# Performance work log

Hardware: AMD Instinct MI355X
Metric: run time of the kernel (lower is better)

The kernel has to match this reference:

```python
import jax, jax.numpy as jnp
import numpy as np

BATCH, D_IN, HID, OUT = 16384, 2000, 100, 2
BN_EPS = 1e-5


def _quant_act(x, bit):
    # HAWQ QuantAct: per-tensor symmetric quantization, returns (dequantized x, scale)
    n = 2 ** (bit - 1) - 1
    s = jnp.max(jnp.abs(x)) / n
    q = jnp.clip(jnp.round(x / s), -n - 1, n)
    return q * s, s


def _quant_linear(x, p_sf, W, b, wbit=2, bbit=2):
    # HAWQ QuantLinear: INT-w GEMM with per-tensor weight scale; bias quantized
    # at scale w_s * p_sf; input assumed pre-quantized at scale p_sf.
    nw = 2 ** (wbit - 1) - 1
    w_s = jnp.max(jnp.abs(W)) / nw
    w_int = jnp.clip(jnp.round(W / w_s), -nw - 1, nw)          # INT2 weights in {-2..1}
    b_s = w_s * p_sf
    nb = 2 ** (bbit - 1)
    b_int = jnp.clip(jnp.round(b / b_s), -nb, nb - 1)
    x_int = x / p_sf                                            # integer-valued activations
    return (x_int @ w_int.T + b_int) * b_s


def setup_inputs() -> dict:
    key = jax.random.key(0)
    ks = jax.random.split(key, 5)
    return {
        "sig": jax.random.normal(ks[0], (BATCH, D_IN), dtype=jnp.float32),
        "W1": jax.random.normal(ks[1], (HID, D_IN), dtype=jnp.float32) * 0.02,
        "b1": jax.random.normal(ks[2], (HID,), dtype=jnp.float32) * 0.01,
        "W2": jax.random.normal(ks[3], (OUT, HID), dtype=jnp.float32) * 0.1,
        "b2": jax.random.normal(ks[4], (OUT,), dtype=jnp.float32) * 0.01,
        "gamma": jnp.ones((HID,), dtype=jnp.float32),
        "beta": jnp.zeros((HID,), dtype=jnp.float32),
    }


def reference(sig, W1, b1, W2, b2, gamma, beta):
    x, p_sf = _quant_act(sig, 5)                    # quant_input (5-bit)
    x = jax.nn.relu(_quant_linear(x, p_sf, W1, b1)) # linear1 (2-bit w/b) + relu
    x, p_sf = _quant_act(x, 8)                      # q_relu1 (8-bit)
    # BatchNorm1d(100) in training mode: batch stats, biased variance
    mu = jnp.mean(x, axis=0)
    var = jnp.mean((x - mu) ** 2, axis=0)
    x = (x - mu) * jax.lax.rsqrt(var + BN_EPS) * gamma + beta
    x = jax.nn.relu(_quant_linear(x, p_sf, W2, b2)) # linear2 (2-bit w/b) + relu
    x, p_sf = _quant_act(x, 8)                      # q_relu2 (8-bit)
    return x
```

## Files before the change

### kernel.cpp

```cpp
#include <hip/hip_runtime.h>
#include <hip/hip_bf16.h>
#include <stdint.h>

#define BATCH   16384
#define D_IN    2000
#define HID     100
#define OUT_DIM 2
#define BN_EPS_VAL 1e-5f

#define BK      32
#define BN_PAD  128
#define KT      63
#define W1Q_ELEMS (KT * BN_PAD * BK)

typedef float f32x4 __attribute__((ext_vector_type(4)));
typedef short bf16x8 __attribute__((ext_vector_type(8)));

#define WS_W1Q_OFF 4096
#define WS_H1_OFF  (1u << 20)
#define WS_Q2_OFF  (8u << 20)
#define WS_O2_OFF  (10u << 20)

__device__ __forceinline__ void block_atomic_maxf(float v, float* dst) {
#pragma unroll
    for (int off = 32; off > 0; off >>= 1)
        v = fmaxf(v, __shfl_xor(v, off, 64));
    __shared__ float sm[8];
    const int w = threadIdx.x >> 6;
    if ((threadIdx.x & 63) == 0) sm[w] = v;
    __syncthreads();
    if (threadIdx.x == 0) {
        const int nw = (blockDim.x + 63) >> 6;
        float m = sm[0];
        for (int i = 1; i < nw; ++i) m = fmaxf(m, sm[i]);
        atomicMax((unsigned int*)dst, __float_as_uint(m));
    }
}

__global__ __launch_bounds__(256)
void k_absmax(const float* __restrict__ sig, const float* __restrict__ W1,
              const float* __restrict__ W2, float* __restrict__ F) {
    float m = 0.0f;
    const int b = blockIdx.x;
    if (b < 2048) {
        const float4* p = (const float4*)sig;
        const int n4 = BATCH * D_IN / 4;
        for (int i = b * 256 + threadIdx.x; i < n4; i += 2048 * 256) {
            float4 v = p[i];
            m = fmaxf(m, fmaxf(fmaxf(fabsf(v.x), fabsf(v.y)),
                               fmaxf(fabsf(v.z), fabsf(v.w))));
        }
        block_atomic_maxf(m, &F[0]);
    } else if (b < 2064) {
        const float4* p = (const float4*)W1;
        const int n4 = HID * D_IN / 4;
        for (int i = (b - 2048) * 256 + threadIdx.x; i < n4; i += 16 * 256) {
            float4 v = p[i];
            m = fmaxf(m, fmaxf(fmaxf(fabsf(v.x), fabsf(v.y)),
                               fmaxf(fabsf(v.z), fabsf(v.w))));
        }
        block_atomic_maxf(m, &F[1]);
    } else {
        if (threadIdx.x < OUT_DIM * HID) m = fabsf(W2[threadIdx.x]);
        block_atomic_maxf(m, &F[2]);
    }
}

__global__ __launch_bounds__(256)
void k_prep(const float* __restrict__ W1, const float* __restrict__ b1,
            const float* __restrict__ W2, float* __restrict__ F,
            unsigned short* __restrict__ w1q) {
    const int tid = blockIdx.x * 256 + threadIdx.x;
    const float ws1 = F[1];
    if (tid < W1Q_ELEMS) {
        const int kt = tid >> 12;
        const int r  = tid & 4095;
        const int n  = r >> 5;
        const int kk = r & 31;
        const int k  = kt * 32 + kk;
        float q = 0.0f;
        if (n < HID && k < D_IN) {
            q = rintf(W1[n * D_IN + k] / ws1);
            q = fminf(fmaxf(q, -2.0f), 1.0f);
        }
        w1q[tid] = (unsigned short)(__float_as_uint(q) >> 16);
    } else if (tid < W1Q_ELEMS + HID) {
        const int h = tid - W1Q_ELEMS;
        const float s1 = F[0] / 15.0f;
        const float bs = ws1 * s1;
        F[16 + h] = fminf(fmaxf(rintf(b1[h] / bs), -2.0f), 1.0f);
    } else if (tid < W1Q_ELEMS + HID + OUT_DIM * HID) {
        const int j = tid - (W1Q_ELEMS + HID);
        const float ws2 = F[2];
        F[116 + j] = fminf(fmaxf(rintf(W2[j] / ws2), -2.0f), 1.0f);
    }
}

__global__ __launch_bounds__(512)
void k_gemm1(const float* __restrict__ sig, const unsigned short* __restrict__ w1q,
             float* __restrict__ F, float* __restrict__ h1) {
    __shared__ float red[4][16][113];
    const int tid  = threadIdx.x;
    const int lane = tid & 63;
    const int wid  = tid >> 6;
    const int rg   = wid & 3;
    const int ks   = wid >> 2;
    const float s1  = F[0] / 15.0f;
    const float bs1 = F[1] * s1;
    const int m0 = blockIdx.x * 64;

    const int fr = lane & 15;
    const int g8 = (lane >> 4) * 8;

    const float* aptr = sig + (size_t)(m0 + rg * 16 + fr) * D_IN;

    f32x4 acc[7] = {};

#pragma unroll 2
    for (int kt = ks; kt < KT; kt += 2) {
        const int k0 = kt * BK + g8;
        float4 va = make_float4(0.f, 0.f, 0.f, 0.f), vb = va;
        if (k0 < D_IN) {
            va = *(const float4*)(aptr + k0);
            vb = *(const float4*)(aptr + k0 + 4);
        }
        union { bf16x8 v; unsigned short s[8]; } A;
        {
            float q;
            q = fminf(fmaxf(rintf(va.x / s1), -16.f), 15.f); A.s[0] = (unsigned short)(__float_as_uint(q) >> 16);
            q = fminf(fmaxf(rintf(va.y / s1), -16.f), 15.f); A.s[1] = (unsigned short)(__float_as_uint(q) >> 16);
            q = fminf(fmaxf(rintf(va.z / s1), -16.f), 15.f); A.s[2] = (unsigned short)(__float_as_uint(q) >> 16);
            q = fminf(fmaxf(rintf(va.w / s1), -16.f), 15.f); A.s[3] = (unsigned short)(__float_as_uint(q) >> 16);
            q = fminf(fmaxf(rintf(vb.x / s1), -16.f), 15.f); A.s[4] = (unsigned short)(__float_as_uint(q) >> 16);
            q = fminf(fmaxf(rintf(vb.y / s1), -16.f), 15.f); A.s[5] = (unsigned short)(__float_as_uint(q) >> 16);
            q = fminf(fmaxf(rintf(vb.z / s1), -16.f), 15.f); A.s[6] = (unsigned short)(__float_as_uint(q) >> 16);
            q = fminf(fmaxf(rintf(vb.w / s1), -16.f), 15.f); A.s[7] = (unsigned short)(__float_as_uint(q) >> 16);
        }
        const unsigned short* bbase = w1q + ((size_t)kt * BN_PAD + fr) * BK + g8;
#pragma unroll
        for (int t = 0; t < 7; ++t) {
            bf16x8 b = *(const bf16x8*)(bbase + t * 16 * BK);
            acc[t] = __builtin_amdgcn_mfma_f32_16x16x32_bf16(A.v, b, acc[t], 0, 0, 0);
        }
    }

    const int rl = (lane >> 4) * 4;
    if (ks == 1) {
#pragma unroll
        for (int t = 0; t < 7; ++t)
#pragma unroll
            for (int r = 0; r < 4; ++r)
                red[rg][rl + r][t * 16 + fr] = acc[t][r];
    }
    __syncthreads();

    float lmax = 0.0f;
    if (ks == 0) {
#pragma unroll
        for (int t = 0; t < 7; ++t) {
            const int n = t * 16 + fr;
            if (n < HID) {
                const float bi = F[16 + n];
#pragma unroll
                for (int r = 0; r < 4; ++r) {
                    const int m = m0 + rg * 16 + rl + r;
                    float h = (acc[t][r] + red[rg][rl + r][n] + bi) * bs1;
                    h = fmaxf(h, 0.0f);
                    h1[(size_t)m * HID + n] = h;
                    lmax = fmaxf(lmax, h);
                }
            }
        }
    }
    block_atomic_maxf(lmax, &F[3]);
}

__global__ __launch_bounds__(256)
void k_quant_h(const float* __restrict__ h1, unsigned char* __restrict__ q2,
               const float* __restrict__ F, unsigned int* __restrict__ S1,
               unsigned int* __restrict__ S2) {
    __shared__ unsigned int ls1[HID], ls2[HID];
    if (threadIdx.x < HID) { ls1[threadIdx.x] = 0u; ls2[threadIdx.x] = 0u; }
    __syncthreads();
    const float s2 = F[3] / 127.0f;
    const int base = blockIdx.x * 25600;
#pragma unroll 4
    for (int it = 0; it < 100; ++it) {
        const int idx = base + it * 256 + threadIdx.x;
        const float h = h1[idx];
        const int q = (int)fminf(rintf(h / s2), 127.0f);
        q2[idx] = (unsigned char)q;
        const int c = idx % HID;
        atomicAdd(&ls1[c], (unsigned int)q);
        atomicAdd(&ls2[c], (unsigned int)(q * q));
    }
    __syncthreads();
    if (threadIdx.x < HID) {
        atomicAdd(&S1[threadIdx.x], ls1[threadIdx.x]);
        atomicAdd(&S2[threadIdx.x], ls2[threadIdx.x]);
    }
}

__global__ void k_bnprep(const float* __restrict__ b2, float* __restrict__ F,
                         const unsigned int* __restrict__ S1,
                         const unsigned int* __restrict__ S2) {
    const int t = threadIdx.x;
    const float s2  = F[3] / 127.0f;
    const float ws2 = F[2];
    const float bs2 = ws2 * s2;
    if (t < HID) {
        const double sd   = (double)s2;
        const double mean = sd * ((double)S1[t] / 16384.0);
        const double ex2  = sd * sd * ((double)S2[t] / 16384.0);
        const double var  = ex2 - mean * mean;
        const float varf  = (float)var;
        const float vpe   = varf + BN_EPS_VAL;
        const float rf    = (float)(1.0 / sqrt((double)vpe));
        F[320 + t] = (float)mean;
        F[420 + t] = rf;
    }
    if (t < OUT_DIM) F[920 + t] = fminf(fmaxf(rintf(b2[t] / bs2), -2.0f), 1.0f);
    if (t == 64) F[922] = bs2;
}

__global__ __launch_bounds__(64)
void k_gemm2(const unsigned char* __restrict__ q2, float* __restrict__ F,
             const float* __restrict__ gamma, const float* __restrict__ beta,
             float* __restrict__ out2) {
    __shared__ float sw[2 * HID], smu[HID], sr[HID], sg[HID], sb[HID];
    __shared__ float ssc[4];
    const int t = threadIdx.x;
    for (int i = t; i < 2 * HID; i += 64) sw[i] = F[116 + i];
    for (int i = t; i < HID; i += 64) {
        smu[i] = F[320 + i]; sr[i] = F[420 + i]; sg[i] = gamma[i]; sb[i] = beta[i];
    }
    if (t == 60) ssc[0] = F[3] / 127.0f;
    if (t == 61) ssc[1] = F[922];
    if (t == 62) ssc[2] = F[920];
    if (t == 63) ssc[3] = F[921];
    __syncthreads();
    const int row = blockIdx.x * 64 + t;
    const unsigned int* rp = (const unsigned int*)(q2 + (size_t)row * HID);
    const float s2 = ssc[0];
    float a0 = 0.0f, a1 = 0.0f;
#pragma unroll
    for (int j = 0; j < 25; ++j) {
        const unsigned int u = rp[j];
#pragma unroll
        for (int bb = 0; bb < 4; ++bb) {
            const int h = j * 4 + bb;
            const float q = (float)((u >> (8 * bb)) & 255u);
            const float x2v = q * s2;
            const float xb  = fmaf((x2v - smu[h]) * sr[h], sg[h], sb[h]);
            const float xi  = xb / s2;
            a0 = fmaf(xi, sw[h], a0);
            a1 = fmaf(xi, sw[HID + h], a1);
        }
    }
    const float o0 = fmaxf((a0 + ssc[2]) * ssc[1], 0.0f);
    const float o1 = fmaxf((a1 + ssc[3]) * ssc[1], 0.0f);
    out2[row * 2 + 0] = o0;
    out2[row * 2 + 1] = o1;
    block_atomic_maxf(fmaxf(o0, o1), &F[4]);
}

__global__ __launch_bounds__(256)
void k_final(const float* __restrict__ out2, const float* __restrict__ F,
             float* __restrict__ out) {
    const int i = blockIdx.x * 256 + threadIdx.x;
    const float s3 = F[4] / 127.0f;
    float4 v = ((const float4*)out2)[i];
    float4 r;
    r.x = fminf(fmaxf(rintf(v.x / s3), -128.f), 127.f) * s3;
    r.y = fminf(fmaxf(rintf(v.y / s3), -128.f), 127.f) * s3;
    r.z = fminf(fmaxf(rintf(v.z / s3), -128.f), 127.f) * s3;
    r.w = fminf(fmaxf(rintf(v.w / s3), -128.f), 127.f) * s3;
    ((float4*)out)[i] = r;
}

extern "C" void kernel_launch(void* const* d_in, const int* in_sizes, int n_in,
                              void* d_out, int out_size, void* d_ws, size_t ws_size,
                              hipStream_t stream) {
    const float* sig   = (const float*)d_in[0];
    const float* W1    = (const float*)d_in[1];
    const float* b1    = (const float*)d_in[2];
    const float* W2    = (const float*)d_in[3];
    const float* b2    = (const float*)d_in[4];
    const float* gamma = (const float*)d_in[5];
    const float* beta  = (const float*)d_in[6];

    float* F = (float*)d_ws;
    unsigned short* w1q = (unsigned short*)((char*)d_ws + WS_W1Q_OFF);
    float* h1           = (float*)((char*)d_ws + WS_H1_OFF);
    unsigned char* q2   = (unsigned char*)((char*)d_ws + WS_Q2_OFF);
    float* o2           = (float*)((char*)d_ws + WS_O2_OFF);
    unsigned int* S1    = (unsigned int*)(F + 520);
    unsigned int* S2    = (unsigned int*)(F + 620);

    hipMemsetAsync(d_ws, 0, 4096, stream);
    k_absmax <<<2065, 256, 0, stream>>>(sig, W1, W2, F);
    k_prep   <<<1010, 256, 0, stream>>>(W1, b1, W2, F, w1q);
    k_gemm1  <<<256,  512, 0, stream>>>(sig, w1q, F, h1);
    k_quant_h<<<64,   256, 0, stream>>>(h1, q2, F, S1, S2);
    k_bnprep <<<1,    128, 0, stream>>>(b2, F, S1, S2);
    k_gemm2  <<<256,  64,  0, stream>>>(q2, F, gamma, beta, o2);
    k_final  <<<32,   256, 0, stream>>>(o2, F, (float*)d_out);
}
```

Before: 315.9 us.

## Regrid GEMM1 with 4-way K split, fuse BN stats finalize into quant kernel

GEMM1 now uses 1024 blocks of 256 threads. Each block covers 16 rows, and its four wavefronts split K four ways, combining partial sums through shared memory. This replaces 256 blocks that each covered 64 rows with a 2-way K split, and the aim is more in-flight memory traffic while streaming the large input. The quant/stats kernel goes from 64 to 256 blocks and writes per-block partial sums. A last-block-done atomic counter then finalizes the BN mean and rstd in place, which removes the separate k_bnprep launch. GEMM2 uses 128-thread blocks. The K bound check on input loads was dropped, so the last tile reads a few floats past the row, and past the end of the buffer for the final row. Those reads multiply zero weights, but that relies on them holding finite values.

```diff
diff --git a/kernel.cpp b/kernel.cpp
--- a/kernel.cpp
+++ b/kernel.cpp
@@ -20,6 +20,8 @@
 #define WS_H1_OFF  (1u << 20)
 #define WS_Q2_OFF  (8u << 20)
 #define WS_O2_OFF  (10u << 20)
+#define WS_P1_OFF  (11u << 20)
+#define WS_P2_OFF  ((11u << 20) + 102400u)
 
 __device__ __forceinline__ void block_atomic_maxf(float v, float* dst) {
 #pragma unroll
@@ -96,34 +98,29 @@
     }
 }
 
-__global__ __launch_bounds__(512)
+__global__ __launch_bounds__(256)
 void k_gemm1(const float* __restrict__ sig, const unsigned short* __restrict__ w1q,
              float* __restrict__ F, float* __restrict__ h1) {
-    __shared__ float red[4][16][113];
+    __shared__ float red[3][16][113];
     const int tid  = threadIdx.x;
     const int lane = tid & 63;
-    const int wid  = tid >> 6;
-    const int rg   = wid & 3;
-    const int ks   = wid >> 2;
+    const int ks   = tid >> 6;
     const float s1  = F[0] / 15.0f;
     const float bs1 = F[1] * s1;
-    const int m0 = blockIdx.x * 64;
+    const int m0 = blockIdx.x * 16;
 
     const int fr = lane & 15;
     const int g8 = (lane >> 4) * 8;
 
-    const float* aptr = sig + (size_t)(m0 + rg * 16 + fr) * D_IN;
+    const float* aptr = sig + (size_t)(m0 + fr) * D_IN;
 
     f32x4 acc[7] = {};
 
 #pragma unroll 2
-    for (int kt = ks; kt < KT; kt += 2) {
+    for (int kt = ks; kt < KT; kt += 4) {
         const int k0 = kt * BK + g8;
-        float4 va = make_float4(0.f, 0.f, 0.f, 0.f), vb = va;
-        if (k0 < D_IN) {
-            va = *(const float4*)(aptr + k0);
-            vb = *(const float4*)(aptr + k0 + 4);
-        }
+        float4 va = *(const float4*)(aptr + k0);
+        float4 vb = *(const float4*)(aptr + k0 + 4);
         union { bf16x8 v; unsigned short s[8]; } A;
         {
             float q;
@@ -145,12 +142,12 @@
     }
 
     const int rl = (lane >> 4) * 4;
-    if (ks == 1) {
+    if (ks != 0) {
 #pragma unroll
         for (int t = 0; t < 7; ++t)
 #pragma unroll
             for (int r = 0; r < 4; ++r)
-                red[rg][rl + r][t * 16 + fr] = acc[t][r];
+                red[ks - 1][rl + r][t * 16 + fr] = acc[t][r];
     }
     __syncthreads();
 
@@ -163,8 +160,9 @@
                 const float bi = F[16 + n];
 #pragma unroll
                 for (int r = 0; r < 4; ++r) {
-                    const int m = m0 + rg * 16 + rl + r;
-                    float h = (acc[t][r] + red[rg][rl + r][n] + bi) * bs1;
+                    const int m = m0 + rl + r;
+                    float h = (acc[t][r] + red[0][rl + r][n] + red[1][rl + r][n]
+                               + red[2][rl + r][n] + bi) * bs1;
                     h = fmaxf(h, 0.0f);
                     h1[(size_t)m * HID + n] = h;
                     lmax = fmaxf(lmax, h);
@@ -177,16 +175,18 @@
 
 __global__ __launch_bounds__(256)
 void k_quant_h(const float* __restrict__ h1, unsigned char* __restrict__ q2,
-               const float* __restrict__ F, unsigned int* __restrict__ S1,
-               unsigned int* __restrict__ S2) {
+               float* __restrict__ F, unsigned int* __restrict__ P1,
+               unsigned int* __restrict__ P2, const float* __restrict__ b2) {
     __shared__ unsigned int ls1[HID], ls2[HID];
-    if (threadIdx.x < HID) { ls1[threadIdx.x] = 0u; ls2[threadIdx.x] = 0u; }
+    __shared__ bool amLast;
+    const int t = threadIdx.x;
+    if (t < HID) { ls1[t] = 0u; ls2[t] = 0u; }
     __syncthreads();
     const float s2 = F[3] / 127.0f;
-    const int base = blockIdx.x * 25600;
-#pragma unroll 4
-    for (int it = 0; it < 100; ++it) {
-        const int idx = base + it * 256 + threadIdx.x;
+    const int base = blockIdx.x * 6400;
+#pragma unroll 5
+    for (int it = 0; it < 25; ++it) {
+        const int idx = base + it * 256 + t;
         const float h = h1[idx];
         const int q = (int)fminf(rintf(h / s2), 127.0f);
         q2[idx] = (unsigned char)q;
@@ -195,23 +195,30 @@
         atomicAdd(&ls2[c], (unsigned int)(q * q));
     }
     __syncthreads();
-    if (threadIdx.x < HID) {
-        atomicAdd(&S1[threadIdx.x], ls1[threadIdx.x]);
-        atomicAdd(&S2[threadIdx.x], ls2[threadIdx.x]);
-    }
-}
-
-__global__ void k_bnprep(const float* __restrict__ b2, float* __restrict__ F,
-                         const unsigned int* __restrict__ S1,
-                         const unsigned int* __restrict__ S2) {
-    const int t = threadIdx.x;
-    const float s2  = F[3] / 127.0f;
-    const float ws2 = F[2];
-    const float bs2 = ws2 * s2;
     if (t < HID) {
+        P1[t * 256 + blockIdx.x] = ls1[t];
+        P2[t * 256 + blockIdx.x] = ls2[t];
+    }
+    __threadfence();
+    if (t == 0) {
+        unsigned int old = atomicAdd((unsigned int*)&F[1000], 1u);
+        amLast = (old == 255u);
+    }
+    __syncthreads();
+    if (!amLast) return;
+    __threadfence();
+    if (t < HID) {
+        const uint4* p1 = (const uint4*)(P1 + t * 256);
+        const uint4* p2 = (const uint4*)(P2 + t * 256);
+        unsigned int s1i = 0u, s2i = 0u;
+#pragma unroll 8
+        for (int j = 0; j < 64; ++j) {
+            uint4 a = p1[j]; s1i += a.x + a.y + a.z + a.w;
+            uint4 b = p2[j]; s2i += b.x + b.y + b.z + b.w;
+        }
         const double sd   = (double)s2;
-        const double mean = sd * ((double)S1[t] / 16384.0);
-        const double ex2  = sd * sd * ((double)S2[t] / 16384.0);
+        const double mean = sd * ((double)s1i / 16384.0);
+        const double ex2  = sd * sd * ((double)s2i / 16384.0);
         const double var  = ex2 - mean * mean;
         const float varf  = (float)var;
         const float vpe   = varf + BN_EPS_VAL;
@@ -219,27 +226,29 @@
         F[320 + t] = (float)mean;
         F[420 + t] = rf;
     }
-    if (t < OUT_DIM) F[920 + t] = fminf(fmaxf(rintf(b2[t] / bs2), -2.0f), 1.0f);
-    if (t == 64) F[922] = bs2;
-}
-
-__global__ __launch_bounds__(64)
+    const float bs2 = F[2] * s2;
+    if (t >= 128 && t < 128 + OUT_DIM)
+        F[920 + (t - 128)] = fminf(fmaxf(rintf(b2[t - 128] / bs2), -2.0f), 1.0f);
+    if (t == 192) F[922] = bs2;
+}
+
+__global__ __launch_bounds__(128)
 void k_gemm2(const unsigned char* __restrict__ q2, float* __restrict__ F,
              const float* __restrict__ gamma, const float* __restrict__ beta,
              float* __restrict__ out2) {
     __shared__ float sw[2 * HID], smu[HID], sr[HID], sg[HID], sb[HID];
     __shared__ float ssc[4];
     const int t = threadIdx.x;
-    for (int i = t; i < 2 * HID; i += 64) sw[i] = F[116 + i];
-    for (int i = t; i < HID; i += 64) {
+    for (int i = t; i < 2 * HID; i += 128) sw[i] = F[116 + i];
+    for (int i = t; i < HID; i += 128) {
         smu[i] = F[320 + i]; sr[i] = F[420 + i]; sg[i] = gamma[i]; sb[i] = beta[i];
     }
-    if (t == 60) ssc[0] = F[3] / 127.0f;
-    if (t == 61) ssc[1] = F[922];
-    if (t == 62) ssc[2] = F[920];
-    if (t == 63) ssc[3] = F[921];
-    __syncthreads();
-    const int row = blockIdx.x * 64 + t;
+    if (t == 120) ssc[0] = F[3] / 127.0f;
+    if (t == 121) ssc[1] = F[922];
+    if (t == 122) ssc[2] = F[920];
+    if (t == 123) ssc[3] = F[921];
+    __syncthreads();
+    const int row = blockIdx.x * 128 + t;
     const unsigned int* rp = (const unsigned int*)(q2 + (size_t)row * HID);
     const float s2 = ssc[0];
     float a0 = 0.0f, a1 = 0.0f;
@@ -294,15 +303,14 @@
     float* h1           = (float*)((char*)d_ws + WS_H1_OFF);
     unsigned char* q2   = (unsigned char*)((char*)d_ws + WS_Q2_OFF);
     float* o2           = (float*)((char*)d_ws + WS_O2_OFF);
-    unsigned int* S1    = (unsigned int*)(F + 520);
-    unsigned int* S2    = (unsigned int*)(F + 620);
+    unsigned int* P1    = (unsigned int*)((char*)d_ws + WS_P1_OFF);
+    unsigned int* P2    = (unsigned int*)((char*)d_ws + WS_P2_OFF);
 
     hipMemsetAsync(d_ws, 0, 4096, stream);
     k_absmax <<<2065, 256, 0, stream>>>(sig, W1, W2, F);
     k_prep   <<<1010, 256, 0, stream>>>(W1, b1, W2, F, w1q);
-    k_gemm1  <<<256,  512, 0, stream>>>(sig, w1q, F, h1);
-    k_quant_h<<<64,   256, 0, stream>>>(h1, q2, F, S1, S2);
-    k_bnprep <<<1,    128, 0, stream>>>(b2, F, S1, S2);
-    k_gemm2  <<<256,  64,  0, stream>>>(q2, F, gamma, beta, o2);
+    k_gemm1  <<<1024, 256, 0, stream>>>(sig, w1q, F, h1);
+    k_quant_h<<<256,  256, 0, stream>>>(h1, q2, F, P1, P2, b2);
+    k_gemm2  <<<128,  128, 0, stream>>>(q2, F, gamma, beta, o2);
     k_final  <<<32,   256, 0, stream>>>(o2, F, (float*)d_out);
 }
```

After: 330.5 us. +4.6%, slower.

## Fuse all stages into one cooperative persistent kernel with grid syncs

Applied to the files above, without the earlier changes.

Replaces the seven-kernel pipeline and memset with a single cooperative kernel of 512 blocks that uses grid.sync between phases: absmax, weight quantization, GEMM1, activation quantization with BN statistics, BN plus GEMM2, and final quantization. The hidden activations stay in shared memory per block instead of round-tripping through global h1/q2/o2 buffers, removing launch overheads and intermediate memory traffic. The GEMM tile shrinks to 32 rows per block with 4 waves. The cost is six grid-wide barriers and lower parallelism in the GEMM and absmax phases, and correctness depends on all 512 blocks being co-resident (2 per CU).

```diff
diff --git a/kernel.cpp b/kernel.cpp
--- a/kernel.cpp
+++ b/kernel.cpp
@@ -1,286 +1,269 @@
 #include <hip/hip_runtime.h>
-#include <hip/hip_bf16.h>
+#include <hip/hip_cooperative_groups.h>
 #include <stdint.h>
+
+namespace cg = cooperative_groups;
 
 #define BATCH   16384
 #define D_IN    2000
 #define HID     100
-#define OUT_DIM 2
 #define BN_EPS_VAL 1e-5f
 
 #define BK      32
 #define BN_PAD  128
 #define KT      63
 #define W1Q_ELEMS (KT * BN_PAD * BK)
+#define NBLK    512
+#define NTHR    256
 
 typedef float f32x4 __attribute__((ext_vector_type(4)));
 typedef short bf16x8 __attribute__((ext_vector_type(8)));
 
 #define WS_W1Q_OFF 4096
-#define WS_H1_OFF  (1u << 20)
-#define WS_Q2_OFF  (8u << 20)
-#define WS_O2_OFF  (10u << 20)
+
+__device__ __forceinline__ unsigned short f2bf(float q) {
+    return (unsigned short)(__float_as_uint(q) >> 16);
+}
 
 __device__ __forceinline__ void block_atomic_maxf(float v, float* dst) {
 #pragma unroll
     for (int off = 32; off > 0; off >>= 1)
         v = fmaxf(v, __shfl_xor(v, off, 64));
-    __shared__ float sm[8];
+    __shared__ float sm[4];
     const int w = threadIdx.x >> 6;
     if ((threadIdx.x & 63) == 0) sm[w] = v;
     __syncthreads();
     if (threadIdx.x == 0) {
-        const int nw = (blockDim.x + 63) >> 6;
-        float m = sm[0];
-        for (int i = 1; i < nw; ++i) m = fmaxf(m, sm[i]);
+        float m = fmaxf(fmaxf(sm[0], sm[1]), fmaxf(sm[2], sm[3]));
         atomicMax((unsigned int*)dst, __float_as_uint(m));
     }
-}
-
-__global__ __launch_bounds__(256)
-void k_absmax(const float* __restrict__ sig, const float* __restrict__ W1,
-              const float* __restrict__ W2, float* __restrict__ F) {
-    float m = 0.0f;
-    const int b = blockIdx.x;
-    if (b < 2048) {
+    __syncthreads();
+}
+
+__global__ __launch_bounds__(NTHR, 2)
+void k_all(const float* __restrict__ sig, const float* __restrict__ W1,
+           const float* __restrict__ b1, const float* __restrict__ W2,
+           const float* __restrict__ b2, const float* __restrict__ gamma,
+           const float* __restrict__ beta, float* __restrict__ F,
+           unsigned short* __restrict__ w1q, float* __restrict__ out) {
+    cg::grid_group grid = cg::this_grid();
+    const int t    = threadIdx.x;
+    const int bid  = blockIdx.x;
+    const int lane = t & 63;
+    const int wid  = t >> 6;
+
+    __shared__ float redf[2][16][113];
+    __shared__ float hbuf[32][104];
+    float* flat = &redf[0][0][0];
+    unsigned int* ls1 = (unsigned int*)flat;
+    unsigned int* ls2 = ls1 + 128;
+    float* sw   = flat + 256;
+    float* smu  = flat + 456;
+    float* sr   = flat + 556;
+    float* sg   = flat + 656;
+    float* sb   = flat + 756;
+    float* ssc  = flat + 856;
+    float* obuf = flat + 864;
+    unsigned int* S1 = (unsigned int*)(F + 520);
+    unsigned int* S2 = (unsigned int*)(F + 620);
+
+    if (bid == 0)
+        for (int i = t; i < 1024; i += NTHR) F[i] = 0.0f;
+    grid.sync();
+
+    {
+        float m = 0.0f;
         const float4* p = (const float4*)sig;
-        const int n4 = BATCH * D_IN / 4;
-        for (int i = b * 256 + threadIdx.x; i < n4; i += 2048 * 256) {
+#pragma unroll 4
+        for (int i = bid * NTHR + t; i < BATCH * D_IN / 4; i += NBLK * NTHR) {
             float4 v = p[i];
             m = fmaxf(m, fmaxf(fmaxf(fabsf(v.x), fabsf(v.y)),
                                fmaxf(fabsf(v.z), fabsf(v.w))));
         }
         block_atomic_maxf(m, &F[0]);
-    } else if (b < 2064) {
-        const float4* p = (const float4*)W1;
-        const int n4 = HID * D_IN / 4;
-        for (int i = (b - 2048) * 256 + threadIdx.x; i < n4; i += 16 * 256) {
-            float4 v = p[i];
-            m = fmaxf(m, fmaxf(fmaxf(fabsf(v.x), fabsf(v.y)),
-                               fmaxf(fabsf(v.z), fabsf(v.w))));
-        }
-        block_atomic_maxf(m, &F[1]);
-    } else {
-        if (threadIdx.x < OUT_DIM * HID) m = fabsf(W2[threadIdx.x]);
-        block_atomic_maxf(m, &F[2]);
-    }
-}
-
-__global__ __launch_bounds__(256)
-void k_prep(const float* __restrict__ W1, const float* __restrict__ b1,
-            const float* __restrict__ W2, float* __restrict__ F,
-            unsigned short* __restrict__ w1q) {
-    const int tid = blockIdx.x * 256 + threadIdx.x;
-    const float ws1 = F[1];
-    if (tid < W1Q_ELEMS) {
-        const int kt = tid >> 12;
-        const int r  = tid & 4095;
-        const int n  = r >> 5;
-        const int kk = r & 31;
-        const int k  = kt * 32 + kk;
-        float q = 0.0f;
-        if (n < HID && k < D_IN) {
-            q = rintf(W1[n * D_IN + k] / ws1);
-            q = fminf(fmaxf(q, -2.0f), 1.0f);
-        }
-        w1q[tid] = (unsigned short)(__float_as_uint(q) >> 16);
-    } else if (tid < W1Q_ELEMS + HID) {
-        const int h = tid - W1Q_ELEMS;
-        const float s1 = F[0] / 15.0f;
-        const float bs = ws1 * s1;
-        F[16 + h] = fminf(fmaxf(rintf(b1[h] / bs), -2.0f), 1.0f);
-    } else if (tid < W1Q_ELEMS + HID + OUT_DIM * HID) {
-        const int j = tid - (W1Q_ELEMS + HID);
-        const float ws2 = F[2];
-        F[116 + j] = fminf(fmaxf(rintf(W2[j] / ws2), -2.0f), 1.0f);
-    }
-}
-
-__global__ __launch_bounds__(512)
-void k_gemm1(const float* __restrict__ sig, const unsigned short* __restrict__ w1q,
-             float* __restrict__ F, float* __restrict__ h1) {
-    __shared__ float red[4][16][113];
-    const int tid  = threadIdx.x;
-    const int lane = tid & 63;
-    const int wid  = tid >> 6;
-    const int rg   = wid & 3;
-    const int ks   = wid >> 2;
-    const float s1  = F[0] / 15.0f;
-    const float bs1 = F[1] * s1;
-    const int m0 = blockIdx.x * 64;
-
-    const int fr = lane & 15;
-    const int g8 = (lane >> 4) * 8;
-
-    const float* aptr = sig + (size_t)(m0 + rg * 16 + fr) * D_IN;
-
-    f32x4 acc[7] = {};
-
+        if (bid < 16) {
+            float mw = 0.0f;
+            const float4* q = (const float4*)W1;
+            for (int i = bid * NTHR + t; i < HID * D_IN / 4; i += 16 * NTHR) {
+                float4 v = q[i];
+                mw = fmaxf(mw, fmaxf(fmaxf(fabsf(v.x), fabsf(v.y)),
+                                     fmaxf(fabsf(v.z), fabsf(v.w))));
+            }
+            block_atomic_maxf(mw, &F[1]);
+        }
+        if (bid == 16) {
+            float mw = (t < 2 * HID) ? fabsf(W2[t]) : 0.0f;
+            block_atomic_maxf(mw, &F[2]);
+        }
+    }
+    grid.sync();
+
+    {
+        const float ws1 = F[1];
+        for (int i = bid * NTHR + t; i < W1Q_ELEMS; i += NBLK * NTHR) {
+            const int kt = i >> 12;
+            const int r  = i & 4095;
+            const int n  = r >> 5;
+            const int kk = r & 31;
+            const int k  = kt * 32 + kk;
+            float qv = 0.0f;
+            if (n < HID && k < D_IN)
+                qv = fminf(fmaxf(rintf(W1[n * D_IN + k] / ws1), -2.0f), 1.0f);
+            w1q[i] = f2bf(qv);
+        }
+        if (bid == 17 && t < HID) {
+            const float bs = ws1 * (F[0] / 15.0f);
+            F[16 + t] = fminf(fmaxf(rintf(b1[t] / bs), -2.0f), 1.0f);
+        }
+        if (bid == 16 && t < 2 * HID)
+            F[116 + t] = fminf(fmaxf(rintf(W2[t] / F[2]), -2.0f), 1.0f);
+    }
+    grid.sync();
+
+    {
+        const float s1  = F[0] / 15.0f;
+        const float bs1 = F[1] * s1;
+        const int m0 = bid * 32;
+        const int rg = wid & 1;
+        const int ks = wid >> 1;
+        const int fr = lane & 15;
+        const int g8 = (lane >> 4) * 8;
+        const float* aptr = sig + (size_t)(m0 + rg * 16 + fr) * D_IN;
+
+        f32x4 acc[7] = {};
 #pragma unroll 2
-    for (int kt = ks; kt < KT; kt += 2) {
-        const int k0 = kt * BK + g8;
-        float4 va = make_float4(0.f, 0.f, 0.f, 0.f), vb = va;
-        if (k0 < D_IN) {
-            va = *(const float4*)(aptr + k0);
-            vb = *(const float4*)(aptr + k0 + 4);
-        }
-        union { bf16x8 v; unsigned short s[8]; } A;
-        {
-            float q;
-            q = fminf(fmaxf(rintf(va.x / s1), -16.f), 15.f); A.s[0] = (unsigned short)(__float_as_uint(q) >> 16);
-            q = fminf(fmaxf(rintf(va.y / s1), -16.f), 15.f); A.s[1] = (unsigned short)(__float_as_uint(q) >> 16);
-            q = fminf(fmaxf(rintf(va.z / s1), -16.f), 15.f); A.s[2] = (unsigned short)(__float_as_uint(q) >> 16);
-            q = fminf(fmaxf(rintf(va.w / s1), -16.f), 15.f); A.s[3] = (unsigned short)(__float_as_uint(q) >> 16);
-            q = fminf(fmaxf(rintf(vb.x / s1), -16.f), 15.f); A.s[4] = (unsigned short)(__float_as_uint(q) >> 16);
-            q = fminf(fmaxf(rintf(vb.y / s1), -16.f), 15.f); A.s[5] = (unsigned short)(__float_as_uint(q) >> 16);
-            q = fminf(fmaxf(rintf(vb.z / s1), -16.f), 15.f); A.s[6] = (unsigned short)(__float_as_uint(q) >> 16);
-            q = fminf(fmaxf(rintf(vb.w / s1), -16.f), 15.f); A.s[7] = (unsigned short)(__float_as_uint(q) >> 16);
-        }
-        const unsigned short* bbase = w1q + ((size_t)kt * BN_PAD + fr) * BK + g8;
-#pragma unroll
-        for (int t = 0; t < 7; ++t) {
-            bf16x8 b = *(const bf16x8*)(bbase + t * 16 * BK);
-            acc[t] = __builtin_amdgcn_mfma_f32_16x16x32_bf16(A.v, b, acc[t], 0, 0, 0);
-        }
-    }
-
-    const int rl = (lane >> 4) * 4;
-    if (ks == 1) {
-#pragma unroll
-        for (int t = 0; t < 7; ++t)
-#pragma unroll
-            for (int r = 0; r < 4; ++r)
-                red[rg][rl + r][t * 16 + fr] = acc[t][r];
-    }
-    __syncthreads();
-
-    float lmax = 0.0f;
-    if (ks == 0) {
-#pragma unroll
-        for (int t = 0; t < 7; ++t) {
-            const int n = t * 16 + fr;
-            if (n < HID) {
-                const float bi = F[16 + n];
-#pragma unroll
-                for (int r = 0; r < 4; ++r) {
-                    const int m = m0 + rg * 16 + rl + r;
-                    float h = (acc[t][r] + red[rg][rl + r][n] + bi) * bs1;
-                    h = fmaxf(h, 0.0f);
-                    h1[(size_t)m * HID + n] = h;
-                    lmax = fmaxf(lmax, h);
+        for (int kt = ks; kt < KT; kt += 2) {
+            const int k0 = kt * BK + g8;
+            union { bf16x8 v; unsigned short s[8]; } A;
+            float e[8];
+            if (k0 + 8 <= D_IN) {
+                float4 va = *(const float4*)(aptr + k0);
+                float4 vb = *(const float4*)(aptr + k0 + 4);
+                e[0]=va.x; e[1]=va.y; e[2]=va.z; e[3]=va.w;
+                e[4]=vb.x; e[5]=vb.y; e[6]=vb.z; e[7]=vb.w;
+            } else {
+#pragma unroll
+                for (int j = 0; j < 8; ++j) e[j] = (k0 + j < D_IN) ? aptr[k0 + j] : 0.0f;
+            }
+#pragma unroll
+            for (int j = 0; j < 8; ++j)
+                A.s[j] = f2bf(fminf(fmaxf(rintf(e[j] / s1), -16.0f), 15.0f));
+
+            const unsigned short* bbase = w1q + ((size_t)kt * BN_PAD + fr) * BK + g8;
+#pragma unroll
+            for (int tt = 0; tt < 7; ++tt) {
+                bf16x8 bfr = *(const bf16x8*)(bbase + tt * 16 * BK);
+                acc[tt] = __builtin_amdgcn_mfma_f32_16x16x32_bf16(A.v, bfr, acc[tt], 0, 0, 0);
+            }
+        }
+
+        const int rl = (lane >> 4) * 4;
+        if (ks == 1) {
+#pragma unroll
+            for (int tt = 0; tt < 7; ++tt)
+#pragma unroll
+                for (int r = 0; r < 4; ++r)
+                    redf[rg][rl + r][tt * 16 + fr] = acc[tt][r];
+        }
+        __syncthreads();
+
+        float lmax = 0.0f;
+        if (ks == 0) {
+#pragma unroll
+            for (int tt = 0; tt < 7; ++tt) {
+                const int n = tt * 16 + fr;
+                if (n < HID) {
+                    const float bi = F[16 + n];
+#pragma unroll
+                    for (int r = 0; r < 4; ++r) {
+                        float h = (acc[tt][r] + redf[rg][rl + r][n] + bi) * bs1;
+                        h = fmaxf(h, 0.0f);
+                        hbuf[rg * 16 + rl + r][n] = h;
+                        lmax = fmaxf(lmax, h);
+                    }
                 }
             }
         }
-    }
-    block_atomic_maxf(lmax, &F[3]);
-}
-
-__global__ __launch_bounds__(256)
-void k_quant_h(const float* __restrict__ h1, unsigned char* __restrict__ q2,
-               const float* __restrict__ F, unsigned int* __restrict__ S1,
-               unsigned int* __restrict__ S2) {
-    __shared__ unsigned int ls1[HID], ls2[HID];
-    if (threadIdx.x < HID) { ls1[threadIdx.x] = 0u; ls2[threadIdx.x] = 0u; }
-    __syncthreads();
-    const float s2 = F[3] / 127.0f;
-    const int base = blockIdx.x * 25600;
-#pragma unroll 4
-    for (int it = 0; it < 100; ++it) {
-        const int idx = base + it * 256 + threadIdx.x;
-        const float h = h1[idx];
-        const int q = (int)fminf(rintf(h / s2), 127.0f);
-        q2[idx] = (unsigned char)q;
-        const int c = idx % HID;
-        atomicAdd(&ls1[c], (unsigned int)q);
-        atomicAdd(&ls2[c], (unsigned int)(q * q));
-    }
-    __syncthreads();
-    if (threadIdx.x < HID) {
-        atomicAdd(&S1[threadIdx.x], ls1[threadIdx.x]);
-        atomicAdd(&S2[threadIdx.x], ls2[threadIdx.x]);
-    }
-}
-
-__global__ void k_bnprep(const float* __restrict__ b2, float* __restrict__ F,
-                         const unsigned int* __restrict__ S1,
-                         const unsigned int* __restrict__ S2) {
-    const int t = threadIdx.x;
-    const float s2  = F[3] / 127.0f;
-    const float ws2 = F[2];
-    const float bs2 = ws2 * s2;
-    if (t < HID) {
-        const double sd   = (double)s2;
-        const double mean = sd * ((double)S1[t] / 16384.0);
-        const double ex2  = sd * sd * ((double)S2[t] / 16384.0);
-        const double var  = ex2 - mean * mean;
-        const float varf  = (float)var;
-        const float vpe   = varf + BN_EPS_VAL;
-        const float rf    = (float)(1.0 / sqrt((double)vpe));
-        F[320 + t] = (float)mean;
-        F[420 + t] = rf;
-    }
-    if (t < OUT_DIM) F[920 + t] = fminf(fmaxf(rintf(b2[t] / bs2), -2.0f), 1.0f);
-    if (t == 64) F[922] = bs2;
-}
-
-__global__ __launch_bounds__(64)
-void k_gemm2(const unsigned char* __restrict__ q2, float* __restrict__ F,
-             const float* __restrict__ gamma, const float* __restrict__ beta,
-             float* __restrict__ out2) {
-    __shared__ float sw[2 * HID], smu[HID], sr[HID], sg[HID], sb[HID];
-    __shared__ float ssc[4];
-    const int t = threadIdx.x;
-    for (int i = t; i < 2 * HID; i += 64) sw[i] = F[116 + i];
-    for (int i = t; i < HID; i += 64) {
-        smu[i] = F[320 + i]; sr[i] = F[420 + i]; sg[i] = gamma[i]; sb[i] = beta[i];
-    }
-    if (t == 60) ssc[0] = F[3] / 127.0f;
-    if (t == 61) ssc[1] = F[922];
-    if (t == 62) ssc[2] = F[920];
-    if (t == 63) ssc[3] = F[921];
-    __syncthreads();
-    const int row = blockIdx.x * 64 + t;
-    const unsigned int* rp = (const unsigned int*)(q2 + (size_t)row * HID);
-    const float s2 = ssc[0];
-    float a0 = 0.0f, a1 = 0.0f;
-#pragma unroll
-    for (int j = 0; j < 25; ++j) {
-        const unsigned int u = rp[j];
-#pragma unroll
-        for (int bb = 0; bb < 4; ++bb) {
-            const int h = j * 4 + bb;
-            const float q = (float)((u >> (8 * bb)) & 255u);
-            const float x2v = q * s2;
-            const float xb  = fmaf((x2v - smu[h]) * sr[h], sg[h], sb[h]);
-            const float xi  = xb / s2;
-            a0 = fmaf(xi, sw[h], a0);
-            a1 = fmaf(xi, sw[HID + h], a1);
-        }
-    }
-    const float o0 = fmaxf((a0 + ssc[2]) * ssc[1], 0.0f);
-    const float o1 = fmaxf((a1 + ssc[3]) * ssc[1], 0.0f);
-    out2[row * 2 + 0] = o0;
-    out2[row * 2 + 1] = o1;
-    block_atomic_maxf(fmaxf(o0, o1), &F[4]);
-}
-
-__global__ __launch_bounds__(256)
-void k_final(const float* __restrict__ out2, const float* __restrict__ F,
-             float* __restrict__ out) {
-    const int i = blockIdx.x * 256 + threadIdx.x;
-    const float s3 = F[4] / 127.0f;
-    float4 v = ((const float4*)out2)[i];
-    float4 r;
-    r.x = fminf(fmaxf(rintf(v.x / s3), -128.f), 127.f) * s3;
-    r.y = fminf(fmaxf(rintf(v.y / s3), -128.f), 127.f) * s3;
-    r.z = fminf(fmaxf(rintf(v.z / s3), -128.f), 127.f) * s3;
-    r.w = fminf(fmaxf(rintf(v.w / s3), -128.f), 127.f) * s3;
-    ((float4*)out)[i] = r;
+        block_atomic_maxf(lmax, &F[3]);
+    }
+    grid.sync();
+
+    {
+        if (t < 128) { ls1[t] = 0u; ls2[t] = 0u; }
+        __syncthreads();
+        const float s2 = F[3] / 127.0f;
+        for (int i = t; i < 32 * HID; i += NTHR) {
+            const int row = i / HID, c = i % HID;
+            const float h = hbuf[row][c];
+            const float q = fminf(rintf(h / s2), 127.0f);
+            hbuf[row][c] = q;
+            const unsigned int qi = (unsigned int)q;
+            atomicAdd(&ls1[c], qi);
+            atomicAdd(&ls2[c], qi * qi);
+        }
+        __syncthreads();
+        if (t < HID) { atomicAdd(&S1[t], ls1[t]); atomicAdd(&S2[t], ls2[t]); }
+    }
+    grid.sync();
+
+    {
+        const float s2 = F[3] / 127.0f;
+        if (t < HID) {
+            const double sd   = (double)s2;
+            const double mean = sd * ((double)S1[t] / 16384.0);
+            const double ex2  = sd * sd * ((double)S2[t] / 16384.0);
+            const double var  = ex2 - mean * mean;
+            const float vpe   = (float)var + BN_EPS_VAL;
+            smu[t] = (float)mean;
+            sr[t]  = (float)(1.0 / sqrt((double)vpe));
+            sg[t]  = gamma[t];
+            sb[t]  = beta[t];
+        }
+        if (t < 2 * HID) sw[t] = F[116 + t];
+        if (t == 220) {
+            const float bs2 = F[2] * s2;
+            ssc[0] = s2;
+            ssc[1] = bs2;
+            ssc[2] = fminf(fmaxf(rintf(b2[0] / bs2), -2.0f), 1.0f);
+            ssc[3] = fminf(fmaxf(rintf(b2[1] / bs2), -2.0f), 1.0f);
+        }
+        __syncthreads();
+
+        float lmax = 0.0f;
+        if (t < 32) {
+            const float s2v = ssc[0];
+            float a0 = 0.0f, a1 = 0.0f;
+            for (int h = 0; h < HID; ++h) {
+                const float q   = hbuf[t][h];
+                const float x2v = q * s2v;
+                const float xb  = fmaf((x2v - smu[h]) * sr[h], sg[h], sb[h]);
+                const float xi  = xb / s2v;
+                a0 = fmaf(xi, sw[h], a0);
+                a1 = fmaf(xi, sw[HID + h], a1);
+            }
+            const float o0 = fmaxf((a0 + ssc[2]) * ssc[1], 0.0f);
+            const float o1 = fmaxf((a1 + ssc[3]) * ssc[1], 0.0f);
+            obuf[t * 2]     = o0;
+            obuf[t * 2 + 1] = o1;
+            lmax = fmaxf(o0, o1);
+        }
+        block_atomic_maxf(lmax, &F[4]);
+    }
+    grid.sync();
+
+    {
+        const float s3 = F[4] / 127.0f;
+        if (t < 64) {
+            const float v = obuf[t];
+            out[bid * 64 + t] = fminf(fmaxf(rintf(v / s3), -128.0f), 127.0f) * s3;
+        }
+    }
 }
 
 extern "C" void kernel_launch(void* const* d_in, const int* in_sizes, int n_in,
                               void* d_out, int out_size, void* d_ws, size_t ws_size,
                               hipStream_t stream) {
+    (void)in_sizes; (void)n_in; (void)out_size; (void)ws_size;
     const float* sig   = (const float*)d_in[0];
     const float* W1    = (const float*)d_in[1];
     const float* b1    = (const float*)d_in[2];
@@ -288,21 +271,11 @@
     const float* b2    = (const float*)d_in[4];
     const float* gamma = (const float*)d_in[5];
     const float* beta  = (const float*)d_in[6];
-
-    float* F = (float*)d_ws;
+    float* F            = (float*)d_ws;
     unsigned short* w1q = (unsigned short*)((char*)d_ws + WS_W1Q_OFF);
-    float* h1           = (float*)((char*)d_ws + WS_H1_OFF);
-    unsigned char* q2   = (unsigned char*)((char*)d_ws + WS_Q2_OFF);
-    float* o2           = (float*)((char*)d_ws + WS_O2_OFF);
-    unsigned int* S1    = (unsigned int*)(F + 520);
-    unsigned int* S2    = (unsigned int*)(F + 620);
-
-    hipMemsetAsync(d_ws, 0, 4096, stream);
-    k_absmax <<<2065, 256, 0, stream>>>(sig, W1, W2, F);
-    k_prep   <<<1010, 256, 0, stream>>>(W1, b1, W2, F, w1q);
-    k_gemm1  <<<256,  512, 0, stream>>>(sig, w1q, F, h1);
-    k_quant_h<<<64,   256, 0, stream>>>(h1, q2, F, S1, S2);
-    k_bnprep <<<1,    128, 0, stream>>>(b2, F, S1, S2);
-    k_gemm2  <<<256,  64,  0, stream>>>(q2, F, gamma, beta, o2);
-    k_final  <<<32,   256, 0, stream>>>(o2, F, (float*)d_out);
-}
+    float* out          = (float*)d_out;
+
+    void* args[] = { &sig, &W1, &b1, &W2, &b2, &gamma, &beta, &F, &w1q, &out };
+    hipLaunchCooperativeKernel((void*)k_all, dim3(NBLK), dim3(NTHR),
+                               args, 0, stream);
+}
```

After: 559.3 us. 1.77x slower.
